# Optimization experiments

Measured on AMD Instinct MI355X. Metric: run time of the kernel, lower is better.

Reference implementation:

```python
import jax, jax.numpy as jnp
import numpy as np

U, I, D = 60000, 90000, 64
N = U + I
NNZ_R, NNZ_S = 1_000_000, 1_000_000
N_RATINGS = 5
RATING_LAYERS = 2
SOCIAL_LAYERS = 2
EMB_COMB = 1.0


def setup_inputs() -> dict:
    key = jax.random.key(0)
    ks = jax.random.split(key, 24)
    inp = {
        'rating_rows': jax.random.randint(ks[0], (N_RATINGS, NNZ_R), 0, N, dtype=jnp.int32),
        'rating_cols': jax.random.randint(ks[1], (N_RATINGS, NNZ_R), 0, N, dtype=jnp.int32),
        'rating_vals': jax.random.uniform(ks[2], (N_RATINGS, NNZ_R), dtype=jnp.float32),
        'friend_rows': jax.random.randint(ks[3], (NNZ_S,), 0, U, dtype=jnp.int32),
        'friend_cols': jax.random.randint(ks[4], (NNZ_S,), 0, U, dtype=jnp.int32),
        'friend_vals': jax.random.uniform(ks[5], (NNZ_S,), dtype=jnp.float32),
        'group_rows': jax.random.randint(ks[6], (NNZ_S,), 0, U, dtype=jnp.int32),
        'group_cols': jax.random.randint(ks[7], (NNZ_S,), 0, U, dtype=jnp.int32),
        'group_vals': jax.random.uniform(ks[8], (NNZ_S,), dtype=jnp.float32),
        'rating_user_emb': jax.random.normal(ks[9], (N_RATINGS, U, D), dtype=jnp.float32) * 0.1,
        'rating_item_emb': jax.random.normal(ks[10], (N_RATINGS, I, D), dtype=jnp.float32) * 0.1,
        'friend_emb': jax.random.normal(ks[11], (U, D), dtype=jnp.float32) * 0.1,
        'group_emb': jax.random.normal(ks[12], (U, D), dtype=jnp.float32) * 0.1,
        'user_att_w': jax.random.normal(ks[13], (D,), dtype=jnp.float32) * 0.1,
        'user_att_mat_w': jax.random.normal(ks[14], (D, D), dtype=jnp.float32) * 0.1,
        'item_att_w': jax.random.normal(ks[15], (D,), dtype=jnp.float32) * 0.1,
        'item_att_mat_w': jax.random.normal(ks[16], (D, D), dtype=jnp.float32) * 0.1,
        'social_att_w': jax.random.normal(ks[17], (D,), dtype=jnp.float32) * 0.1,
        'social_att_mat_w': jax.random.normal(ks[18], (D, D), dtype=jnp.float32) * 0.1,
        'adaptive_emb_comb': jax.random.uniform(ks[19], (U,), dtype=jnp.float32) + 0.5,
    }
    return inp


def _spmm(rows, cols, vals, x, n):
    # COO sparse matmul: out[r] += vals[e] * x[cols[e]]
    return jax.ops.segment_sum(vals[:, None] * x[cols], rows, num_segments=n)


def _l2norm(x):
    # F.normalize(x, p=2, dim=1)
    return x / jnp.clip(jnp.linalg.norm(x, axis=1, keepdims=True), 1e-12)


def _att_fuse(embs, a, M):
    # embs: [C, N, D]; weight[c,n] = tanh((emb @ M.T) @ a); softmax over channels C
    w = jnp.tanh(jnp.einsum('cnd,ed,e->cn', embs, M, a))
    scores = jax.nn.softmax(w, axis=0)  # [C, N]
    mixed = jnp.einsum('cn,cnd->nd', scores, embs)
    return mixed, scores


def reference(rating_rows, rating_cols, rating_vals,
              friend_rows, friend_cols, friend_vals,
              group_rows, group_cols, group_vals,
              rating_user_emb, rating_item_emb, friend_emb, group_emb,
              user_att_w, user_att_mat_w, item_att_w, item_att_mat_w,
              social_att_w, social_att_mat_w, adaptive_emb_comb):
    # ---- rating channels: LightGCN propagation over bipartite graph ----
    user_list, item_list = [], []
    for c in range(N_RATINGS):
        ego = jnp.concatenate([rating_user_emb[c], rating_item_emb[c]], axis=0)  # [N, D]
        layers = []
        for _ in range(RATING_LAYERS):
            ego = _spmm(rating_rows[c], rating_cols[c], rating_vals[c], ego, N)
            layers.append(ego)
        mean_emb = jnp.mean(jnp.stack(layers, axis=0), axis=0)
        user_list.append(mean_emb[:U])
        item_list.append(mean_emb[U:])
    user_embs = jnp.stack(user_list, axis=0)  # [C, U, D]
    item_embs = jnp.stack(item_list, axis=0)  # [C, I, D]
    mixed_rating_user, user_scores = _att_fuse(user_embs, user_att_w, user_att_mat_w)
    mixed_rating_item, item_scores = _att_fuse(item_embs, item_att_w, item_att_mat_w)

    # ---- social channels: propagation + per-layer L2 normalize ----
    def social_prop(rows, cols, vals, emb):
        outs = []
        for _ in range(SOCIAL_LAYERS):
            emb = _l2norm(_spmm(rows, cols, vals, emb, U))
            outs.append(emb)
        return jnp.mean(jnp.stack(outs, axis=0), axis=0)

    friend_u = social_prop(friend_rows, friend_cols, friend_vals, friend_emb)
    group_u = social_prop(group_rows, group_cols, group_vals, group_emb)
    social_embs = jnp.stack([friend_u, group_u], axis=0)  # [2, U, D]
    mixed_social, social_scores = _att_fuse(social_embs, social_att_w, social_att_mat_w)

    # ---- adaptive combination ----
    num = jnp.sum(mixed_rating_user * mixed_social, axis=1)
    denom = (jnp.clip(jnp.linalg.norm(mixed_rating_user, axis=1), 1e-8)
             * jnp.clip(jnp.linalg.norm(mixed_social, axis=1), 1e-8))
    emb_sim = num / denom
    emb_sim_up_0 = jnp.maximum(emb_sim, 0.0)
    base = (SOCIAL_LAYERS + RATING_LAYERS) / 2.0
    rate = EMB_COMB / (base + emb_sim_up_0 * adaptive_emb_comb)[:, None]  # [U, 1]
    mixed_user = mixed_rating_user + mixed_social * rate
    return (user_scores, item_scores, social_scores, mixed_user, mixed_rating_item)
```

## Files before the change

### kernel.cpp

```cpp
#include <hip/hip_runtime.h>
#include <hip/hip_bf16.h>

#define UU 60000
#define II 90000
#define DD 64
#define NN 150000
#define NNZC 1000000
#define NTOT 7000000
#define MTOT 870000
#define ROW_S0 750000
#define NBR 733
#define NBCK 1046
#define CAPE 8192
#define ACH 16384
#define GRID_A 428
#define ABLK 1024

struct SpmmJob {
    int mode;
    int rowBase;
    int nRows;
    const uint2* tblB;
    const uint2* selfB;
    uint2* outB;
    float4* outF;
    float* wOut;
};

struct CvtJob {
    const float* lo;
    const float* hi;
    uint2* dst;
    int nRows;
    int split;
};

__device__ __forceinline__ int wave_incl_scan(int x) {
    int lane = threadIdx.x & 63;
#pragma unroll
    for (int d = 1; d < 64; d <<= 1) {
        int y = __shfl_up(x, d, 64);
        if (lane >= d) x += y;
    }
    return x;
}

__device__ int block_incl_scan(int x, int* lds) {
    int wid = threadIdx.x >> 6, lane = threadIdx.x & 63;
    int ws_ = wave_incl_scan(x);
    if (lane == 63) lds[wid] = ws_;
    __syncthreads();
    int off = 0;
    for (int w = 0; w < wid; ++w) off += lds[w];
    __syncthreads();
    return ws_ + off;
}

__device__ __forceinline__ float2 unpack_bf16x2(unsigned p) {
    float2 r;
    r.x = __uint_as_float(p << 16);
    r.y = __uint_as_float(p & 0xffff0000u);
    return r;
}

__device__ __forceinline__ unsigned pack_bf16x2(float a, float b) {
    __hip_bfloat162 h = __float22bfloat162_rn(make_float2(a, b));
    return *(unsigned*)&h;
}

__device__ __forceinline__ uint2 pack4(float4 m) {
    return make_uint2(pack_bf16x2(m.x, m.y), pack_bf16x2(m.z, m.w));
}

__device__ __forceinline__ float4 unpack4(uint2 p) {
    float2 a = unpack_bf16x2(p.x), b = unpack_bf16x2(p.y);
    return make_float4(a.x, a.y, b.x, b.y);
}

__device__ __forceinline__ int bid_of(int grow) {
    return (grow < ROW_S0) ? (grow >> 10) : NBR + (grow - ROW_S0) / 384;
}

__device__ __forceinline__ void cvt_body(int blk, int nblks, const CvtJob& cv) {
    int total = cv.nRows * 16;
    int stride = nblks * (int)blockDim.x;
    for (int i = blk * (int)blockDim.x + (int)threadIdx.x; i < total; i += stride) {
        int row = i >> 4, h = i & 15;
        const float* src = (row < cv.split) ? (cv.lo + (size_t)row * DD)
                                            : (cv.hi + (size_t)(row - cv.split) * DD);
        float4 x = *(const float4*)(src + 4 * h);
        cv.dst[i] = pack4(x);
    }
}

__global__ void att_vec_kernel(const float* __restrict__ au, const float* __restrict__ Mu,
                               const float* __restrict__ ai, const float* __restrict__ Mi,
                               const float* __restrict__ as_, const float* __restrict__ Ms,
                               float* __restrict__ v) {
    int d = threadIdx.x;
    float su = 0.f, si = 0.f, ss = 0.f;
    for (int e = 0; e < DD; ++e) {
        su += au[e] * Mu[e * DD + d];
        si += ai[e] * Mi[e * DD + d];
        ss += as_[e] * Ms[e * DD + d];
    }
    v[d] = su;
    v[DD + d] = si;
    v[2 * DD + d] = ss;
}

__device__ __forceinline__ void decode_full(int e, const int* __restrict__ rR,
                                            const int* __restrict__ rC, const float* __restrict__ rV,
                                            const int* __restrict__ fR, const int* __restrict__ fC,
                                            const float* __restrict__ fV,
                                            const int* __restrict__ gR, const int* __restrict__ gC,
                                            const float* __restrict__ gV,
                                            int& grow, int& c, float& v) {
    if (e < 5 * NNZC) { grow = (e / NNZC) * NN + rR[e]; c = rC[e]; v = rV[e]; }
    else if (e < 6 * NNZC) { int k = e - 5 * NNZC; grow = ROW_S0 + fR[k]; c = fC[k]; v = fV[k]; }
    else { int k = e - 6 * NNZC; grow = ROW_S0 + UU + gR[k]; c = gC[k]; v = gV[k]; }
}

__global__ __launch_bounds__(ABLK) void pa_single_kernel(
        const int* __restrict__ rR, const int* __restrict__ rC, const float* __restrict__ rV,
        const int* __restrict__ fR, const int* __restrict__ fC, const float* __restrict__ fV,
        const int* __restrict__ gR, const int* __restrict__ gC, const float* __restrict__ gV,
        int* __restrict__ bucketCur, uint2* __restrict__ ecv) {
    __shared__ int lcnt[NBCK];
    __shared__ int lbase[NBCK];
    int k = blockIdx.x;
    int cbase = k * ACH;
    int eEnd = min(cbase + ACH, NTOT);
    for (int b = threadIdx.x; b < NBCK; b += ABLK) lcnt[b] = 0;
    __syncthreads();
    for (int e0 = cbase + threadIdx.x; e0 < eEnd; e0 += 4 * ABLK) {
        int gw[4]; bool val[4];
#pragma unroll
        for (int u = 0; u < 4; ++u) {
            int e = e0 + u * ABLK;
            val[u] = e < eEnd;
            int ec = val[u] ? e : cbase;
            if (ec < 5 * NNZC) gw[u] = (ec / NNZC) * NN + rR[ec];
            else if (ec < 6 * NNZC) gw[u] = ROW_S0 + fR[ec - 5 * NNZC];
            else gw[u] = ROW_S0 + UU + gR[ec - 6 * NNZC];
        }
#pragma unroll
        for (int u = 0; u < 4; ++u)
            if (val[u]) atomicAdd(&lcnt[bid_of(gw[u])], 1);
    }
    __syncthreads();
    for (int b = threadIdx.x; b < NBCK; b += ABLK) {
        int n = lcnt[b];
        lbase[b] = n ? atomicAdd(&bucketCur[b], n) : 0;
    }
    __syncthreads();
    for (int b = threadIdx.x; b < NBCK; b += ABLK) lcnt[b] = 0;
    __syncthreads();
    for (int e0 = cbase + threadIdx.x; e0 < eEnd; e0 += 4 * ABLK) {
        int gw[4], cc[4]; float vv[4]; bool val[4];
#pragma unroll
        for (int u = 0; u < 4; ++u) {
            int e = e0 + u * ABLK;
            val[u] = e < eEnd;
            int ec = val[u] ? e : cbase;
            decode_full(ec, rR, rC, rV, fR, fC, fV, gR, gC, gV, gw[u], cc[u], vv[u]);
        }
        int rk[4], bb[4];
#pragma unroll
        for (int u = 0; u < 4; ++u) {
            bb[u] = bid_of(gw[u]);
            rk[u] = val[u] ? atomicAdd(&lcnt[bb[u]], 1) : 0;
        }
#pragma unroll
        for (int u = 0; u < 4; ++u) {
            if (!val[u]) continue;
            int off = lbase[bb[u]] + rk[u];
            if (off >= CAPE) continue;
            int lrow = (gw[u] < ROW_S0) ? (gw[u] & 1023) : ((gw[u] - ROW_S0) % 384);
            ecv[(size_t)bb[u] * CAPE + off] =
                make_uint2(((unsigned)lrow << 18) | (unsigned)cc[u], __float_as_uint(vv[u]));
        }
    }
}

__global__ __launch_bounds__(256) void bscan_kernel(const int* __restrict__ bucketCur,
                                                    int* __restrict__ bStart,
                                                    int* __restrict__ rowptr,
                                                    CvtJob cv, int cvB) {
    if (blockIdx.x > 0) {
        cvt_body(blockIdx.x - 1, cvB, cv);
        return;
    }
    __shared__ int lds8[8];
    __shared__ int sOff;
    if (threadIdx.x == 0) sOff = 0;
    __syncthreads();
    for (int base = 0; base < NBCK; base += 256) {
        int i = base + threadIdx.x;
        int v = (i < NBCK) ? min(bucketCur[i], CAPE) : 0;
        int incl = block_incl_scan(v, lds8);
        if (i < NBCK) bStart[i] = sOff + incl - v;
        __syncthreads();
        if (threadIdx.x == 255) sOff += incl;
        __syncthreads();
    }
    if (threadIdx.x == 0) { bStart[NBCK] = sOff; rowptr[MTOT] = sOff; }
}

__global__ __launch_bounds__(256) void phaseB_kernel(const int* __restrict__ bStart,
                                                     const int* __restrict__ bucketCur,
                                                     int* __restrict__ rowptr,
                                                     const uint2* __restrict__ ecv,
                                                     uint2* __restrict__ edata,
                                                     CvtJob cv, int cvB) {
    if ((int)blockIdx.x >= NBCK) {
        cvt_body(blockIdx.x - NBCK, cvB, cv);
        return;
    }
    __shared__ unsigned short perm[CAPE];
    __shared__ int off[1024];
    __shared__ int lds8[8];
    int b = blockIdx.x;
    int firstRow = (b < NBR) ? (b << 10) : ROW_S0 + (b - NBR) * 384;
    int rowEnd = (b < NBR) ? min((b + 1) << 10, ROW_S0)
                           : min(ROW_S0 + (b - NBR + 1) * 384, MTOT);
    int nRows = rowEnd - firstRow;
    size_t src = (size_t)b * CAPE;
    int dst = bStart[b];
    int count = min(bucketCur[b], CAPE);
    for (int i = threadIdx.x; i < nRows; i += 256) off[i] = 0;
    __syncthreads();
    for (int i = threadIdx.x; i < count; i += 256)
        atomicAdd(&off[ecv[src + i].x >> 18], 1);
    __syncthreads();
    int base4 = threadIdx.x * 4;
    int v4[4], s = 0;
#pragma unroll
    for (int kk = 0; kk < 4; ++kk) {
        int i = base4 + kk;
        v4[kk] = (i < nRows) ? off[i] : 0;
        s += v4[kk];
    }
    int incl = block_incl_scan(s, lds8);
    int run = incl - s;
#pragma unroll
    for (int kk = 0; kk < 4; ++kk) {
        int i = base4 + kk;
        if (i < nRows) { rowptr[firstRow + i] = dst + run; off[i] = run; }
        run += v4[kk];
    }
    __syncthreads();
    for (int i = threadIdx.x; i < count; i += 256) {
        int pos = atomicAdd(&off[ecv[src + i].x >> 18], 1);
        perm[pos] = (unsigned short)i;
    }
    __syncthreads();
    for (int i = threadIdx.x; i < count; i += 256) {
        uint2 e = ecv[src + perm[i]];
        edata[dst + i] = make_uint2(e.x & 0x3FFFFu, e.y);
    }
}

template <int MODE>
__device__ __forceinline__ void spmm_body(int blk, const SpmmJob& j,
                                          const int* __restrict__ rowptr,
                                          const uint2* __restrict__ edata,
                                          const float* __restrict__ vvec) {
    int lane = threadIdx.x & 63;
    int l16 = lane & 15;
    int grpBase = lane & 48;
    int wid = blk * (int)(blockDim.x >> 6) + (threadIdx.x >> 6);
    int row = wid * 4 + (lane >> 4);
    bool active = row < j.nRows;
    int g = j.rowBase + row;
    int start = active ? rowptr[g] : 0;
    int end = active ? rowptr[g + 1] : 0;
    float4 acc = make_float4(0.f, 0.f, 0.f, 0.f);
    for (int j0 = start; j0 < end; j0 += 16) {
        uint2 md = make_uint2(0u, 0u);
        if (j0 + l16 < end) md = edata[j0 + l16];
        int cnt = min(end - j0, 16);
        for (int js = 0; js < cnt; js += 8) {
            int cc[8]; float vv[8]; float4 xv[8];
#pragma unroll
            for (int u = 0; u < 8; ++u) {
                int jj = js + u;
                int sl = grpBase + ((jj < cnt) ? jj : 0);
                cc[u] = __shfl((int)md.x, sl, 64);
                float v = __uint_as_float((unsigned)__shfl((int)md.y, sl, 64));
                vv[u] = (jj < cnt) ? v : 0.f;
            }
#pragma unroll
            for (int u = 0; u < 8; ++u)
                xv[u] = unpack4(j.tblB[(size_t)cc[u] * 16 + l16]);
#pragma unroll
            for (int u = 0; u < 8; ++u) {
                acc.x += vv[u] * xv[u].x; acc.y += vv[u] * xv[u].y;
                acc.z += vv[u] * xv[u].z; acc.w += vv[u] * xv[u].w;
            }
        }
    }
    if (!active) return;
    size_t ro = (size_t)row * 16 + l16;
    if (MODE == 0) {
        j.outB[ro] = pack4(acc);
    } else if (MODE == 1) {
        float4 sv = unpack4(j.selfB[ro]);
        float4 m = make_float4(0.5f * (acc.x + sv.x), 0.5f * (acc.y + sv.y),
                               0.5f * (acc.z + sv.z), 0.5f * (acc.w + sv.w));
        j.outB[ro] = pack4(m);
        const float* vv = (row < UU) ? vvec : (vvec + DD);
        float4 vw = *(const float4*)(vv + 4 * l16);
        float p = m.x * vw.x + m.y * vw.y + m.z * vw.z + m.w * vw.w;
        p += __shfl_xor(p, 1, 64); p += __shfl_xor(p, 2, 64);
        p += __shfl_xor(p, 4, 64); p += __shfl_xor(p, 8, 64);
        if (l16 == 0) j.wOut[row] = tanhf(p);
    } else if (MODE == 2) {
        float n2 = acc.x * acc.x + acc.y * acc.y + acc.z * acc.z + acc.w * acc.w;
        n2 += __shfl_xor(n2, 1, 64); n2 += __shfl_xor(n2, 2, 64);
        n2 += __shfl_xor(n2, 4, 64); n2 += __shfl_xor(n2, 8, 64);
        float inv = 1.f / fmaxf(sqrtf(n2), 1e-12f);
        j.outB[ro] = pack4(make_float4(acc.x * inv, acc.y * inv, acc.z * inv, acc.w * inv));
    } else {
        float n2 = acc.x * acc.x + acc.y * acc.y + acc.z * acc.z + acc.w * acc.w;
        n2 += __shfl_xor(n2, 1, 64); n2 += __shfl_xor(n2, 2, 64);
        n2 += __shfl_xor(n2, 4, 64); n2 += __shfl_xor(n2, 8, 64);
        float inv = 1.f / fmaxf(sqrtf(n2), 1e-12f);
        float4 sv = unpack4(j.selfB[ro]);
        j.outF[ro] = make_float4(0.5f * (sv.x + acc.x * inv), 0.5f * (sv.y + acc.y * inv),
                                 0.5f * (sv.z + acc.z * inv), 0.5f * (sv.w + acc.w * inv));
    }
}

__device__ __forceinline__ void spmm_run(const SpmmJob& j, int blk,
                                         const int* __restrict__ rowptr,
                                         const uint2* __restrict__ edata,
                                         const float* __restrict__ vvec) {
    switch (j.mode) {
        case 0: spmm_body<0>(blk, j, rowptr, edata, vvec); break;
        case 1: spmm_body<1>(blk, j, rowptr, edata, vvec); break;
        case 2: spmm_body<2>(blk, j, rowptr, edata, vvec); break;
        default: spmm_body<3>(blk, j, rowptr, edata, vvec); break;
    }
}

__global__ __launch_bounds__(256) void fused_kernel(SpmmJob a, int aB, SpmmJob b, int bB,
                                                    CvtJob cv, int cvB,
                                                    const int* __restrict__ rowptr,
                                                    const uint2* __restrict__ edata,
                                                    const float* __restrict__ vvec) {
    int bx = blockIdx.x;
    if (bx < aB) { spmm_run(a, bx, rowptr, edata, vvec); return; }
    bx -= aB;
    if (bx < bB) { spmm_run(b, bx, rowptr, edata, vvec); return; }
    cvt_body(bx - bB, cvB, cv);
}

__global__ void mix5_kernel(const __hip_bfloat16* __restrict__ chanEmb,
                            const float* __restrict__ w,
                            float* __restrict__ oUS, float* __restrict__ oIS,
                            float* __restrict__ mixedRU, float* __restrict__ oMI) {
    int lane = threadIdx.x & 63;
    int n = blockIdx.x * (blockDim.x >> 6) + (threadIdx.x >> 6);
    if (n >= NN) return;
    float sw[5];
    float mx = -2.0f;
#pragma unroll
    for (int c = 0; c < 5; ++c) {
        sw[c] = w[(size_t)c * NN + n];
        mx = fmaxf(mx, sw[c]);
    }
    float sum = 0.f;
#pragma unroll
    for (int c = 0; c < 5; ++c) {
        sw[c] = expf(sw[c] - mx);
        sum += sw[c];
    }
    float inv = 1.0f / sum;
    float acc = 0.f;
#pragma unroll
    for (int c = 0; c < 5; ++c) {
        sw[c] *= inv;
        acc += sw[c] * __bfloat162float(chanEmb[((size_t)c * NN + n) * DD + lane]);
    }
    if (n < UU) {
#pragma unroll
        for (int c = 0; c < 5; ++c)
            if (lane == c) oUS[(size_t)c * UU + n] = sw[c];
        mixedRU[(size_t)n * DD + lane] = acc;
    } else {
        int m = n - UU;
#pragma unroll
        for (int c = 0; c < 5; ++c)
            if (lane == c) oIS[(size_t)c * II + m] = sw[c];
        oMI[(size_t)m * DD + lane] = acc;
    }
}

__global__ void social_mix_final_kernel(const float* __restrict__ e0, const float* __restrict__ e1,
                                        const float* __restrict__ vs,
                                        const float* __restrict__ mixedRU,
                                        const float* __restrict__ adaptive,
                                        float* __restrict__ scoresOut,
                                        float* __restrict__ outMU) {
    int lane = threadIdx.x & 63;
    int n = blockIdx.x * (blockDim.x >> 6) + (threadIdx.x >> 6);
    if (n >= UU) return;
    size_t idx = (size_t)n * DD + lane;
    float a = e0[idx];
    float b = e1[idx];
    float v = vs[lane];
    float pa = a * v, pb = b * v;
    float mru = mixedRU[idx];
#pragma unroll
    for (int m = 32; m >= 1; m >>= 1) { pa += __shfl_xor(pa, m, 64); pb += __shfl_xor(pb, m, 64); }
    float w0 = tanhf(pa);
    float w1 = tanhf(pb);
    float mx = fmaxf(w0, w1);
    float x0 = expf(w0 - mx);
    float x1 = expf(w1 - mx);
    float invs = 1.0f / (x0 + x1);
    float s0 = x0 * invs;
    float s1 = x1 * invs;
    if (lane == 0) {
        scoresOut[n] = s0;
        scoresOut[UU + n] = s1;
    }
    float ms = s0 * a + s1 * b;
    float nm = mru * ms, na2 = mru * mru, nb2 = ms * ms;
#pragma unroll
    for (int m = 32; m >= 1; m >>= 1) {
        nm += __shfl_xor(nm, m, 64); na2 += __shfl_xor(na2, m, 64); nb2 += __shfl_xor(nb2, m, 64);
    }
    float denom = fmaxf(sqrtf(na2), 1e-8f) * fmaxf(sqrtf(nb2), 1e-8f);
    float sim = nm / denom;
    float rate = 1.0f / (2.0f + fmaxf(sim, 0.f) * adaptive[n]);
    outMU[idx] = mru + ms * rate;
}

extern "C" void kernel_launch(void* const* d_in, const int* in_sizes, int n_in,
                              void* d_out, int out_size, void* d_ws, size_t ws_size,
                              hipStream_t stream) {
    const int* r_rows = (const int*)d_in[0];
    const int* r_cols = (const int*)d_in[1];
    const float* r_vals = (const float*)d_in[2];
    const int* f_rows = (const int*)d_in[3];
    const int* f_cols = (const int*)d_in[4];
    const float* f_vals = (const float*)d_in[5];
    const int* g_rows = (const int*)d_in[6];
    const int* g_cols = (const int*)d_in[7];
    const float* g_vals = (const float*)d_in[8];
    const float* rue = (const float*)d_in[9];
    const float* rie = (const float*)d_in[10];
    const float* femb = (const float*)d_in[11];
    const float* gemb = (const float*)d_in[12];
    const float* uaw = (const float*)d_in[13];
    const float* uamw = (const float*)d_in[14];
    const float* iaw = (const float*)d_in[15];
    const float* iamw = (const float*)d_in[16];
    const float* saw = (const float*)d_in[17];
    const float* samw = (const float*)d_in[18];
    const float* adapt = (const float*)d_in[19];

    float* ws = (float*)d_ws;
    int* rowptr = (int*)ws;
    int* bStart = rowptr + 870016;
    int* bucketCur = bStart + 2048;
    float* ED   = ws + 874112;
    float* R1   = ED + 14000000;
    float* CM   = R1 + 11520000;
    float* tbl0F= CM + 24000000;
    float* wrat = tbl0F + 4800000;
    float* vvec = wrat + 750016;

    uint2* edata = (uint2*)ED;
    uint2* AtmpB0 = (uint2*)R1;
    uint2* AtmpB1 = AtmpB0 + (size_t)NN * 16;
    float* mixedRU = R1;
    float* socM0 = R1 + 3840000;
    float* socM1 = R1 + 7680000;
    uint2* ecv = (uint2*)CM;
    __hip_bfloat16* chanMean = (__hip_bfloat16*)CM;
    uint2* tbl1 = (uint2*)(CM + 19200000);
    uint2* socL1B0 = (uint2*)CM;
    uint2* socL1B1 = (uint2*)(CM + 1920000);
    uint2* tbl0 = (uint2*)tbl0F;
    uint2* socB0 = (uint2*)tbl0F;
    uint2* socB1 = socB0 + (size_t)UU * 16;

    float* out = (float*)d_out;
    float* oUS = out;
    float* oIS = oUS + (size_t)5 * UU;
    float* oSS = oIS + (size_t)5 * II;
    float* oMU = oSS + (size_t)2 * UU;
    float* oMI = oMU + (size_t)UU * DD;

    const dim3 blk(256);
    const dim3 blkA(ABLK);
    const int gridN4 = (NN + 15) / 16;
    const int gridU4 = (UU + 15) / 16;
    const int gridMix = (NN + 3) / 4;
    const int gridFin = (UU + 3) / 4;
    const int CVB = 2048;

    uint2* tblOf[2] = {tbl0, tbl1};
    auto cvtRating = [&](int c) {
        CvtJob cv{};
        cv.lo = rue + (size_t)c * UU * DD;
        cv.hi = rie + (size_t)c * II * DD;
        cv.dst = tblOf[c & 1];
        cv.nRows = NN; cv.split = UU;
        return cv;
    };
    CvtJob cvNone{};
    cvNone.lo = rue; cvNone.hi = rie; cvNone.dst = tbl0; cvNone.nRows = 0; cvNone.split = UU;

    att_vec_kernel<<<1, 64, 0, stream>>>(uaw, uamw, iaw, iamw, saw, samw, vvec);

    hipMemsetAsync(bucketCur, 0, NBCK * sizeof(int), stream);
    pa_single_kernel<<<GRID_A, blkA, 0, stream>>>(r_rows, r_cols, r_vals,
                                                  f_rows, f_cols, f_vals,
                                                  g_rows, g_cols, g_vals,
                                                  bucketCur, ecv);
    bscan_kernel<<<1 + CVB, blk, 0, stream>>>(bucketCur, bStart, rowptr,
                                              cvtRating(0), CVB);
    phaseB_kernel<<<NBCK + CVB, blk, 0, stream>>>(bStart, bucketCur, rowptr, ecv, edata,
                                                  cvtRating(1), CVB);

    auto jobL1 = [&](int c) {
        SpmmJob j{};
        j.mode = 0; j.rowBase = c * NN; j.nRows = NN;
        j.tblB = tblOf[c & 1];
        j.outB = (c & 1) ? AtmpB1 : AtmpB0;
        return j;
    };
    auto jobL2 = [&](int c) {
        SpmmJob j{};
        j.mode = 1; j.rowBase = c * NN; j.nRows = NN;
        j.tblB = (c & 1) ? AtmpB1 : AtmpB0;
        j.selfB = j.tblB;
        j.outB = (uint2*)(chanMean + (size_t)c * NN * DD);
        j.wOut = wrat + (size_t)c * NN;
        return j;
    };
    SpmmJob jNone{}; jNone.mode = 0; jNone.nRows = 0; jNone.tblB = tbl0; jNone.outB = AtmpB0;

    fused_kernel<<<gridN4, blk, 0, stream>>>(jobL1(0), gridN4, jNone, 0, cvNone, 0,
                                             rowptr, edata, vvec);
    for (int c = 1; c <= 3; ++c)
        fused_kernel<<<2 * gridN4 + CVB, blk, 0, stream>>>(
            jobL1(c), gridN4, jobL2(c - 1), gridN4, cvtRating(c + 1), CVB,
            rowptr, edata, vvec);
    fused_kernel<<<2 * gridN4, blk, 0, stream>>>(jobL1(4), gridN4, jobL2(3), gridN4,
                                                 cvNone, 0, rowptr, edata, vvec);
    CvtJob cvSoc{};
    cvSoc.lo = femb; cvSoc.hi = gemb; cvSoc.dst = socB0; cvSoc.nRows = 2 * UU; cvSoc.split = UU;
    fused_kernel<<<gridN4 + CVB, blk, 0, stream>>>(jobL2(4), gridN4, jNone, 0, cvSoc, CVB,
                                                   rowptr, edata, vvec);

    mix5_kernel<<<gridMix, blk, 0, stream>>>(chanMean, wrat, oUS, oIS, mixedRU, oMI);

    SpmmJob sf1{}; sf1.mode = 2; sf1.rowBase = ROW_S0; sf1.nRows = UU;
    sf1.tblB = socB0; sf1.outB = socL1B0;
    SpmmJob sg1{}; sg1.mode = 2; sg1.rowBase = ROW_S0 + UU; sg1.nRows = UU;
    sg1.tblB = socB1; sg1.outB = socL1B1;
    fused_kernel<<<2 * gridU4, blk, 0, stream>>>(sf1, gridU4, sg1, gridU4, cvNone, 0,
                                                 rowptr, edata, vvec);

    SpmmJob sf2{}; sf2.mode = 3; sf2.rowBase = ROW_S0; sf2.nRows = UU;
    sf2.tblB = socL1B0; sf2.selfB = socL1B0; sf2.outF = (float4*)socM0;
    SpmmJob sg2{}; sg2.mode = 3; sg2.rowBase = ROW_S0 + UU; sg2.nRows = UU;
    sg2.tblB = socL1B1; sg2.selfB = socL1B1; sg2.outF = (float4*)socM1;
    fused_kernel<<<2 * gridU4, blk, 0, stream>>>(sf2, gridU4, sg2, gridU4, cvNone, 0,
                                                 rowptr, edata, vvec);

    social_mix_final_kernel<<<gridFin, blk, 0, stream>>>(socM0, socM1, vvec + 2 * DD,
                                                         mixedRU, adapt, oSS, oMU);
}
```

Baseline: 579.3 us.

## Fuse attention-vector, mix5 and social layer-1 SpMM into existing launches

The separate attention-vector kernel now runs as an extra block of the bucket-scan kernel. The mix5 kernel and the first social SpMM layer share one launch, with the social layer-1 buffers moved into the mixed-user output region so they no longer alias the channel-mean buffer. The bucketing kernel keeps the 16 decoded row ids per thread in registers so the second pass does not reload row indices. Together these cut launch count and redundant index loads, at the cost of more register pressure and of depending on the output buffer being overwritten later.

```diff
diff --git a/kernel.cpp b/kernel.cpp
--- a/kernel.cpp
+++ b/kernel.cpp
@@ -93,34 +93,6 @@
     }
 }
 
-__global__ void att_vec_kernel(const float* __restrict__ au, const float* __restrict__ Mu,
-                               const float* __restrict__ ai, const float* __restrict__ Mi,
-                               const float* __restrict__ as_, const float* __restrict__ Ms,
-                               float* __restrict__ v) {
-    int d = threadIdx.x;
-    float su = 0.f, si = 0.f, ss = 0.f;
-    for (int e = 0; e < DD; ++e) {
-        su += au[e] * Mu[e * DD + d];
-        si += ai[e] * Mi[e * DD + d];
-        ss += as_[e] * Ms[e * DD + d];
-    }
-    v[d] = su;
-    v[DD + d] = si;
-    v[2 * DD + d] = ss;
-}
-
-__device__ __forceinline__ void decode_full(int e, const int* __restrict__ rR,
-                                            const int* __restrict__ rC, const float* __restrict__ rV,
-                                            const int* __restrict__ fR, const int* __restrict__ fC,
-                                            const float* __restrict__ fV,
-                                            const int* __restrict__ gR, const int* __restrict__ gC,
-                                            const float* __restrict__ gV,
-                                            int& grow, int& c, float& v) {
-    if (e < 5 * NNZC) { grow = (e / NNZC) * NN + rR[e]; c = rC[e]; v = rV[e]; }
-    else if (e < 6 * NNZC) { int k = e - 5 * NNZC; grow = ROW_S0 + fR[k]; c = fC[k]; v = fV[k]; }
-    else { int k = e - 6 * NNZC; grow = ROW_S0 + UU + gR[k]; c = gC[k]; v = gV[k]; }
-}
-
 __global__ __launch_bounds__(ABLK) void pa_single_kernel(
         const int* __restrict__ rR, const int* __restrict__ rC, const float* __restrict__ rV,
         const int* __restrict__ fR, const int* __restrict__ fC, const float* __restrict__ fV,
@@ -133,21 +105,21 @@
     int eEnd = min(cbase + ACH, NTOT);
     for (int b = threadIdx.x; b < NBCK; b += ABLK) lcnt[b] = 0;
     __syncthreads();
-    for (int e0 = cbase + threadIdx.x; e0 < eEnd; e0 += 4 * ABLK) {
-        int gw[4]; bool val[4];
-#pragma unroll
-        for (int u = 0; u < 4; ++u) {
-            int e = e0 + u * ABLK;
-            val[u] = e < eEnd;
-            int ec = val[u] ? e : cbase;
-            if (ec < 5 * NNZC) gw[u] = (ec / NNZC) * NN + rR[ec];
-            else if (ec < 6 * NNZC) gw[u] = ROW_S0 + fR[ec - 5 * NNZC];
-            else gw[u] = ROW_S0 + UU + gR[ec - 6 * NNZC];
-        }
-#pragma unroll
-        for (int u = 0; u < 4; ++u)
-            if (val[u]) atomicAdd(&lcnt[bid_of(gw[u])], 1);
-    }
+    int gw[16];
+#pragma unroll
+    for (int t = 0; t < 16; ++t) {
+        int e = cbase + t * ABLK + (int)threadIdx.x;
+        bool v = e < eEnd;
+        int ec = v ? e : cbase;
+        int grow;
+        if (ec < 5 * NNZC) grow = (ec / NNZC) * NN + rR[ec];
+        else if (ec < 6 * NNZC) grow = ROW_S0 + fR[ec - 5 * NNZC];
+        else grow = ROW_S0 + UU + gR[ec - 6 * NNZC];
+        gw[t] = v ? grow : -1;
+    }
+#pragma unroll
+    for (int t = 0; t < 16; ++t)
+        if (gw[t] >= 0) atomicAdd(&lcnt[bid_of(gw[t])], 1);
     __syncthreads();
     for (int b = threadIdx.x; b < NBCK; b += ABLK) {
         int n = lcnt[b];
@@ -156,27 +128,32 @@
     __syncthreads();
     for (int b = threadIdx.x; b < NBCK; b += ABLK) lcnt[b] = 0;
     __syncthreads();
-    for (int e0 = cbase + threadIdx.x; e0 < eEnd; e0 += 4 * ABLK) {
-        int gw[4], cc[4]; float vv[4]; bool val[4];
+#pragma unroll
+    for (int t0 = 0; t0 < 16; t0 += 4) {
+        int cc[4]; float vv[4];
 #pragma unroll
         for (int u = 0; u < 4; ++u) {
-            int e = e0 + u * ABLK;
-            val[u] = e < eEnd;
-            int ec = val[u] ? e : cbase;
-            decode_full(ec, rR, rC, rV, fR, fC, fV, gR, gC, gV, gw[u], cc[u], vv[u]);
+            int t = t0 + u;
+            int e = cbase + t * ABLK + (int)threadIdx.x;
+            int ec = (gw[t] >= 0) ? e : cbase;
+            if (ec < 5 * NNZC) { cc[u] = rC[ec]; vv[u] = rV[ec]; }
+            else if (ec < 6 * NNZC) { int kk = ec - 5 * NNZC; cc[u] = fC[kk]; vv[u] = fV[kk]; }
+            else { int kk = ec - 6 * NNZC; cc[u] = gC[kk]; vv[u] = gV[kk]; }
         }
         int rk[4], bb[4];
 #pragma unroll
         for (int u = 0; u < 4; ++u) {
-            bb[u] = bid_of(gw[u]);
-            rk[u] = val[u] ? atomicAdd(&lcnt[bb[u]], 1) : 0;
+            int t = t0 + u;
+            bb[u] = (gw[t] >= 0) ? bid_of(gw[t]) : 0;
+            rk[u] = (gw[t] >= 0) ? atomicAdd(&lcnt[bb[u]], 1) : CAPE;
         }
 #pragma unroll
         for (int u = 0; u < 4; ++u) {
-            if (!val[u]) continue;
+            int t = t0 + u;
+            if (gw[t] < 0) continue;
             int off = lbase[bb[u]] + rk[u];
             if (off >= CAPE) continue;
-            int lrow = (gw[u] < ROW_S0) ? (gw[u] & 1023) : ((gw[u] - ROW_S0) % 384);
+            int lrow = (gw[t] < ROW_S0) ? (gw[t] & 1023) : ((gw[t] - ROW_S0) % 384);
             ecv[(size_t)bb[u] * CAPE + off] =
                 make_uint2(((unsigned)lrow << 18) | (unsigned)cc[u], __float_as_uint(vv[u]));
         }
@@ -186,7 +163,29 @@
 __global__ __launch_bounds__(256) void bscan_kernel(const int* __restrict__ bucketCur,
                                                     int* __restrict__ bStart,
                                                     int* __restrict__ rowptr,
-                                                    CvtJob cv, int cvB) {
+                                                    CvtJob cv, int cvB,
+                                                    const float* __restrict__ au,
+                                                    const float* __restrict__ Mu,
+                                                    const float* __restrict__ ai,
+                                                    const float* __restrict__ Mi,
+                                                    const float* __restrict__ as_,
+                                                    const float* __restrict__ Ms,
+                                                    float* __restrict__ vvec) {
+    if ((int)blockIdx.x == 1 + cvB) {
+        int d = threadIdx.x;
+        if (d < DD) {
+            float su = 0.f, si = 0.f, ss = 0.f;
+            for (int e = 0; e < DD; ++e) {
+                su += au[e] * Mu[e * DD + d];
+                si += ai[e] * Mi[e * DD + d];
+                ss += as_[e] * Ms[e * DD + d];
+            }
+            vvec[d] = su;
+            vvec[DD + d] = si;
+            vvec[2 * DD + d] = ss;
+        }
+        return;
+    }
     if (blockIdx.x > 0) {
         cvt_body(blockIdx.x - 1, cvB, cv);
         return;
@@ -356,12 +355,21 @@
     cvt_body(bx - bB, cvB, cv);
 }
 
-__global__ void mix5_kernel(const __hip_bfloat16* __restrict__ chanEmb,
-                            const float* __restrict__ w,
-                            float* __restrict__ oUS, float* __restrict__ oIS,
-                            float* __restrict__ mixedRU, float* __restrict__ oMI) {
+__global__ __launch_bounds__(256) void mix_social_kernel(
+        const __hip_bfloat16* __restrict__ chanEmb, const float* __restrict__ w,
+        float* __restrict__ oUS, float* __restrict__ oIS,
+        float* __restrict__ mixedRU, float* __restrict__ oMI, int nMix,
+        SpmmJob s0, int s0B, SpmmJob s1,
+        const int* __restrict__ rowptr, const uint2* __restrict__ edata,
+        const float* __restrict__ vvec) {
+    if ((int)blockIdx.x >= nMix) {
+        int r = blockIdx.x - nMix;
+        if (r < s0B) spmm_body<2>(r, s0, rowptr, edata, vvec);
+        else spmm_body<2>(r - s0B, s1, rowptr, edata, vvec);
+        return;
+    }
     int lane = threadIdx.x & 63;
-    int n = blockIdx.x * (blockDim.x >> 6) + (threadIdx.x >> 6);
+    int n = blockIdx.x * 4 + (threadIdx.x >> 6);
     if (n >= NN) return;
     float sw[5];
     float mx = -2.0f;
@@ -482,8 +490,6 @@
     uint2* ecv = (uint2*)CM;
     __hip_bfloat16* chanMean = (__hip_bfloat16*)CM;
     uint2* tbl1 = (uint2*)(CM + 19200000);
-    uint2* socL1B0 = (uint2*)CM;
-    uint2* socL1B1 = (uint2*)(CM + 1920000);
     uint2* tbl0 = (uint2*)tbl0F;
     uint2* socB0 = (uint2*)tbl0F;
     uint2* socB1 = socB0 + (size_t)UU * 16;
@@ -494,6 +500,8 @@
     float* oSS = oIS + (size_t)5 * II;
     float* oMU = oSS + (size_t)2 * UU;
     float* oMI = oMU + (size_t)UU * DD;
+    uint2* socL1B0 = (uint2*)oMU;
+    uint2* socL1B1 = socL1B0 + (size_t)UU * 16;
 
     const dim3 blk(256);
     const dim3 blkA(ABLK);
@@ -515,15 +523,14 @@
     CvtJob cvNone{};
     cvNone.lo = rue; cvNone.hi = rie; cvNone.dst = tbl0; cvNone.nRows = 0; cvNone.split = UU;
 
-    att_vec_kernel<<<1, 64, 0, stream>>>(uaw, uamw, iaw, iamw, saw, samw, vvec);
-
     hipMemsetAsync(bucketCur, 0, NBCK * sizeof(int), stream);
     pa_single_kernel<<<GRID_A, blkA, 0, stream>>>(r_rows, r_cols, r_vals,
                                                   f_rows, f_cols, f_vals,
                                                   g_rows, g_cols, g_vals,
                                                   bucketCur, ecv);
-    bscan_kernel<<<1 + CVB, blk, 0, stream>>>(bucketCur, bStart, rowptr,
-                                              cvtRating(0), CVB);
+    bscan_kernel<<<2 + CVB, blk, 0, stream>>>(bucketCur, bStart, rowptr,
+                                              cvtRating(0), CVB,
+                                              uaw, uamw, iaw, iamw, saw, samw, vvec);
     phaseB_kernel<<<NBCK + CVB, blk, 0, stream>>>(bStart, bucketCur, rowptr, ecv, edata,
                                                   cvtRating(1), CVB);
 
@@ -558,14 +565,13 @@
     fused_kernel<<<gridN4 + CVB, blk, 0, stream>>>(jobL2(4), gridN4, jNone, 0, cvSoc, CVB,
                                                    rowptr, edata, vvec);
 
-    mix5_kernel<<<gridMix, blk, 0, stream>>>(chanMean, wrat, oUS, oIS, mixedRU, oMI);
-
     SpmmJob sf1{}; sf1.mode = 2; sf1.rowBase = ROW_S0; sf1.nRows = UU;
     sf1.tblB = socB0; sf1.outB = socL1B0;
     SpmmJob sg1{}; sg1.mode = 2; sg1.rowBase = ROW_S0 + UU; sg1.nRows = UU;
     sg1.tblB = socB1; sg1.outB = socL1B1;
-    fused_kernel<<<2 * gridU4, blk, 0, stream>>>(sf1, gridU4, sg1, gridU4, cvNone, 0,
-                                                 rowptr, edata, vvec);
+    mix_social_kernel<<<gridMix + 2 * gridU4, blk, 0, stream>>>(
+        chanMean, wrat, oUS, oIS, mixedRU, oMI, gridMix,
+        sf1, gridU4, sg1, rowptr, edata, vvec);
 
     SpmmJob sf2{}; sf2.mode = 3; sf2.rowBase = ROW_S0; sf2.nRows = UU;
     sf2.tblB = socL1B0; sf2.selfB = socL1B0; sf2.outF = (float4*)socM0;
```

Measured after the change: 593.9 us. 1.03x slower.
